# Kernel optimization log

Measured on AMD Instinct MI355X. Metric: run time of the kernel, lower is better.

The kernel has to match this reference:

```python
import jax, jax.numpy as jnp
import numpy as np

D_MODEL = 1024
N_HEAD = 16
D_HEAD = 64


def setup_inputs() -> dict:
    key = jax.random.key(0)
    k1, k2, k3 = jax.random.split(key, 3)
    B, T = 2, 2048
    x = jax.random.normal(k1, (B, T, D_MODEL), dtype=jnp.float32)
    # Linear weights (scaled like typical init to keep softmax numerics sane)
    w_attn = jax.random.normal(k2, (D_MODEL, 3 * D_MODEL), dtype=jnp.float32) * (1.0 / np.sqrt(D_MODEL))
    w_proj = jax.random.normal(k3, (D_MODEL, D_MODEL), dtype=jnp.float32) * (1.0 / np.sqrt(D_MODEL))
    return {"x": x, "w_attn": w_attn, "w_proj": w_proj}


def reference(x, w_attn, w_proj):
    B, T, C = x.shape
    # c_attn: fused qkv projection (use_bias=False)
    qkv = jnp.einsum('btc,cf->btf', x, w_attn)  # [B, T, 3C]
    q, k, v = jnp.split(qkv, 3, axis=-1)
    q = q.reshape(B, T, N_HEAD, D_HEAD)
    k = k.reshape(B, T, N_HEAD, D_HEAD)
    v = v.reshape(B, T, N_HEAD, D_HEAD)
    # scaled QK^T with causal mask (cache=None training path)
    att = jnp.einsum('bqhd,bkhd->bhqk', q, k) * (1.0 / jnp.sqrt(jnp.float32(D_HEAD)))
    causal = jnp.tril(jnp.ones((T, T), dtype=bool))  # [T, T]
    att = jnp.where(causal[None, None, :, :], att, -jnp.inf)
    att = jax.nn.softmax(att, axis=-1)
    # dropout is a no-op (deterministic / p=0)
    y = jnp.einsum('bhqk,bkhd->bqhd', att, v).reshape(B, T, C)
    y = jnp.einsum('btc,cd->btd', y, w_proj)
    return y
```

## Files before the change

kernel.cpp:

```cpp
#include <hip/hip_runtime.h>
#include <hip/hip_bf16.h>


typedef __attribute__((ext_vector_type(8))) __bf16 bf16x8;
typedef __attribute__((ext_vector_type(4))) float  floatx4;
typedef __attribute__((ext_vector_type(4))) float  fvec4;
typedef __attribute__((ext_vector_type(4))) short  short4v;

#define MFMA16(a, b, c) __builtin_amdgcn_mfma_f32_16x16x32_bf16(a, b, c, 0, 0, 0)

using as1v = const __attribute__((address_space(1))) void;
using as3v = __attribute__((address_space(3))) void;
__device__ __forceinline__ void async16(const void* g, void* l) {
  __builtin_amdgcn_global_load_lds((as1v*)g, (as3v*)l, 16, 0, 0);
}

__device__ inline void store_out(float* p, float v) { *p = v; }
__device__ inline void store_out(__hip_bfloat16* p, float v) { *p = __float2bfloat16(v); }

__global__ __launch_bounds__(256) void prep_kernel(const float* __restrict__ x,
                                                   const float* __restrict__ w_attn,
                                                   const float* __restrict__ w_proj,
                                                   __hip_bfloat16* __restrict__ xb,
                                                   __hip_bfloat16* __restrict__ wat,
                                                   __hip_bfloat16* __restrict__ wpt) {
  __shared__ float tile[32][33];
  const int bid = blockIdx.x, tid = threadIdx.x;
  if (bid < 4096) {
    const int i = (bid * 256 + tid) * 4;
    fvec4 v = *(const fvec4*)(x + i);
    union { short4v s; __hip_bfloat16 h[4]; } u;
#pragma unroll
    for (int j = 0; j < 4; ++j) u.h[j] = __float2bfloat16(v[j]);
    *(short4v*)((short*)xb + i) = u.s;
    return;
  }
  const float* in;
  __hip_bfloat16* out;
  int rows, cols, bx, by;
  if (bid < 4096 + 3072) {
    const int b2 = bid - 4096;
    in = w_attn; out = wat; rows = 1024; cols = 3072; bx = b2 % 96; by = b2 / 96;
  } else {
    const int b2 = bid - 7168;
    in = w_proj; out = wpt; rows = 1024; cols = 1024; bx = b2 % 32; by = b2 / 32;
  }
  const int tx = tid & 31, ty = tid >> 5;
  const int c0 = bx * 32, r0 = by * 32;
#pragma unroll
  for (int i = 0; i < 32; i += 8)
    tile[ty + i][tx] = in[(long)(r0 + ty + i) * cols + c0 + tx];
  __syncthreads();
#pragma unroll
  for (int i = 0; i < 32; i += 8)
    out[(long)(c0 + ty + i) * rows + r0 + tx] = __float2bfloat16(tile[tx][ty + i]);
}

__global__ __launch_bounds__(256) void vt_kernel(const __hip_bfloat16* __restrict__ qkv,
                                                 __hip_bfloat16* __restrict__ vt) {
  __shared__ __align__(16) __hip_bfloat16 tile[64 * 64];
  const int tid = threadIdx.x;
  const int tt0 = blockIdx.x * 64, h = blockIdx.y, b = blockIdx.z;
  const long bh = (long)b * 16 + h;
#pragma unroll
  for (int it = 0; it < 2; ++it) {
    const int c = it * 256 + tid;
    const int row = c >> 3, cg = c & 7;
    const int pg = cg ^ ((row >> 3) & 7);
    *(bf16x8*)(tile + row * 64 + pg * 8) =
        *(const bf16x8*)(qkv + ((long)b * 2048 + tt0 + row) * 3072 + 2048 + h * 64 + cg * 8);
  }
  __syncthreads();
#pragma unroll
  for (int it = 0; it < 2; ++it) {
    const int c = it * 256 + tid;
    const int dr = c >> 3, tg = c & 7;
    union { bf16x8 v; __hip_bfloat16 e[8]; } u;
    const int pg = (dr >> 3) ^ tg;
#pragma unroll
    for (int j = 0; j < 8; ++j)
      u.e[j] = tile[(tg * 8 + j) * 64 + pg * 8 + (dr & 7)];
    *(bf16x8*)(vt + (bh * 64 + dr) * 2048 + tt0 + tg * 8) = u.v;
  }
}

template <typename OutT>
__global__ __launch_bounds__(256) void gemm_bt_kernel(const __hip_bfloat16* __restrict__ A,
                                                      const __hip_bfloat16* __restrict__ Bt,
                                                      OutT* __restrict__ C,
                                                      int M, int N, int K,
                                                      float qscale, int qlim) {
  __shared__ __align__(16) __hip_bfloat16 As[2][128 * 32];
  __shared__ __align__(16) __hip_bfloat16 Bs[2][128 * 32];
  const int tid = threadIdx.x;
  const int lane = tid & 63, wv = tid >> 6;
  const int l15 = lane & 15, quad = lane >> 4;
  const int wm = wv >> 1, wn = wv & 1;
  const long m0 = (long)blockIdx.y * 128, n0 = (long)blockIdx.x * 128;
  floatx4 acc[4][4] = {};
  const int nk = K >> 5;

  auto issue = [&](int kt, int p) {
    const int k0 = kt << 5;
#pragma unroll
    for (int it = 0; it < 2; ++it) {
      const int c = it * 256 + tid;
      const int row = c >> 2;
      const int lcg = (c & 3) ^ ((row >> 1) & 3);
      async16(A + (m0 + row) * K + k0 + lcg * 8, (char*)&As[p][0] + c * 16);
      async16(Bt + (n0 + row) * K + k0 + lcg * 8, (char*)&Bs[p][0] + c * 16);
    }
  };

  issue(0, 0);
  for (int kt = 0; kt < nk; ++kt) {
    const int p = kt & 1;
    __syncthreads();
    if (kt + 1 < nk) issue(kt + 1, p ^ 1);
    bf16x8 af[4], bfr[4];
#pragma unroll
    for (int t = 0; t < 4; ++t) {
      const int ar = wm * 64 + t * 16 + l15;
      const int br = wn * 64 + t * 16 + l15;
      af[t]  = *(const bf16x8*)(&As[p][ar * 32 + (quad ^ ((ar >> 1) & 3)) * 8]);
      bfr[t] = *(const bf16x8*)(&Bs[p][br * 32 + (quad ^ ((br >> 1) & 3)) * 8]);
    }
#pragma unroll
    for (int mt = 0; mt < 4; ++mt)
#pragma unroll
      for (int nt = 0; nt < 4; ++nt)
        acc[mt][nt] = MFMA16(af[mt], bfr[nt], acc[mt][nt]);
  }
#pragma unroll
  for (int mt = 0; mt < 4; ++mt)
#pragma unroll
    for (int nt = 0; nt < 4; ++nt)
#pragma unroll
      for (int r = 0; r < 4; ++r) {
        const long row = m0 + wm * 64 + mt * 16 + quad * 4 + r;
        const long col = n0 + wn * 64 + nt * 16 + l15;
        float v = acc[mt][nt][r];
        if ((int)col < qlim) v *= qscale;
        store_out(C + row * N + col, v);
      }
}

template <typename OutT>
__global__ __launch_bounds__(256) void gemm_bt64_kernel(const __hip_bfloat16* __restrict__ A,
                                                        const __hip_bfloat16* __restrict__ Bt,
                                                        OutT* __restrict__ C,
                                                        int M, int N, int K) {
  __shared__ __align__(16) __hip_bfloat16 As[2][128 * 32];
  __shared__ __align__(16) __hip_bfloat16 Bs[2][64 * 32];
  const int tid = threadIdx.x;
  const int lane = tid & 63, wv = tid >> 6;
  const int l15 = lane & 15, quad = lane >> 4;
  const int wm = wv >> 1, wn = wv & 1;
  const long m0 = (long)blockIdx.y * 128, n0 = (long)blockIdx.x * 64;
  floatx4 acc[4][2] = {};
  const int nk = K >> 5;

  auto issue = [&](int kt, int p) {
    const int k0 = kt << 5;
#pragma unroll
    for (int it = 0; it < 2; ++it) {
      const int c = it * 256 + tid;
      const int row = c >> 2;
      const int lcg = (c & 3) ^ ((row >> 1) & 3);
      async16(A + (m0 + row) * K + k0 + lcg * 8, (char*)&As[p][0] + c * 16);
    }
    {
      const int c = tid;
      const int row = c >> 2;
      const int lcg = (c & 3) ^ ((row >> 1) & 3);
      async16(Bt + (n0 + row) * K + k0 + lcg * 8, (char*)&Bs[p][0] + c * 16);
    }
  };

  issue(0, 0);
  for (int kt = 0; kt < nk; ++kt) {
    const int p = kt & 1;
    __syncthreads();
    if (kt + 1 < nk) issue(kt + 1, p ^ 1);
    bf16x8 af[4], bfr[2];
#pragma unroll
    for (int t = 0; t < 4; ++t) {
      const int ar = wm * 64 + t * 16 + l15;
      af[t] = *(const bf16x8*)(&As[p][ar * 32 + (quad ^ ((ar >> 1) & 3)) * 8]);
    }
#pragma unroll
    for (int t = 0; t < 2; ++t) {
      const int br = wn * 32 + t * 16 + l15;
      bfr[t] = *(const bf16x8*)(&Bs[p][br * 32 + (quad ^ ((br >> 1) & 3)) * 8]);
    }
#pragma unroll
    for (int mt = 0; mt < 4; ++mt)
#pragma unroll
      for (int nt = 0; nt < 2; ++nt)
        acc[mt][nt] = MFMA16(af[mt], bfr[nt], acc[mt][nt]);
  }
#pragma unroll
  for (int mt = 0; mt < 4; ++mt)
#pragma unroll
    for (int nt = 0; nt < 2; ++nt)
#pragma unroll
      for (int r = 0; r < 4; ++r) {
        const long row = m0 + wm * 64 + mt * 16 + quad * 4 + r;
        const long col = n0 + wn * 32 + nt * 16 + l15;
        store_out(C + row * N + col, acc[mt][nt][r]);
      }
}

__global__ __launch_bounds__(256) void attn_kernel(const __hip_bfloat16* __restrict__ qkv,
                                                   const __hip_bfloat16* __restrict__ vtg,
                                                   __hip_bfloat16* __restrict__ y) {
  __shared__ __align__(16) __hip_bfloat16 Ks[2][64 * 64];
  __shared__ __align__(16) __hip_bfloat16 Vt[2][64 * 64];
  __shared__ __align__(16) __hip_bfloat16 Pb[4][16 * 64];
  const int tid = threadIdx.x;
  const int lane = tid & 63, wv = tid >> 6;
  const int l15 = lane & 15, quad = lane >> 4;
  const int pt = blockIdx.x, h = blockIdx.y, b = blockIdx.z;
  const int qtA = pt, qtB = 31 - pt;
  const int q0A = qtA * 64, q0B = qtB * 64;
  const long bh = (long)b * 16 + h;
  const long RS = 3072;

  auto issue = [&](int kt, int p) {
    const int kb = kt * 64;
#pragma unroll
    for (int it = 0; it < 2; ++it) {
      const int c = it * 256 + tid;
      const int row = c >> 3;
      const int cg = (c & 7) ^ (row & 7);
      async16(qkv + ((long)b * 2048 + kb + row) * RS + 1024 + h * 64 + cg * 8,
              (char*)&Ks[p][0] + c * 16);
      async16(vtg + (bh * 64 + row) * 2048 + kb + cg * 8, (char*)&Vt[p][0] + c * 16);
    }
  };

  bf16x8 bqA0, bqA1, bqB0, bqB1;
  {
    const __hip_bfloat16* qpA = qkv + ((long)b * 2048 + q0A + wv * 16 + l15) * RS + h * 64 + quad * 8;
    bqA0 = *(const bf16x8*)qpA;
    bqA1 = *(const bf16x8*)(qpA + 32);
    const __hip_bfloat16* qpB = qkv + ((long)b * 2048 + q0B + wv * 16 + l15) * RS + h * 64 + quad * 8;
    bqB0 = *(const bf16x8*)qpB;
    bqB1 = *(const bf16x8*)(qpB + 32);
  }
  union { bf16x8 v; __hip_bfloat16 e[8]; } uo;
#pragma unroll
  for (int j = 0; j < 8; ++j) uo.e[j] = __float2bfloat16(1.0f);
  const bf16x8 ones = uo.v;

  floatx4 oA[4] = {}, oB[4] = {}, o4A = {}, o4B = {};
  __hip_bfloat16* Pw = &Pb[wv][0];
  const int m7 = l15 & 7;

  issue(0, 0);
  for (int kt = 0; kt <= qtB; ++kt) {
    const int p = kt & 1;
    const int kb = kt * 64;
    const bool actA = (kt <= qtA);
    __syncthreads();
    if (kt < qtB) issue(kt + 1, p ^ 1);

    bf16x8 kf[4][2], vf[4][2];
#pragma unroll
    for (int nt = 0; nt < 4; ++nt) {
      const int row = nt * 16 + l15;
      const int s0 = (quad ^ (row & 7)) * 8, s1 = ((quad + 4) ^ (row & 7)) * 8;
      kf[nt][0] = *(const bf16x8*)(&Ks[p][row * 64 + s0]);
      kf[nt][1] = *(const bf16x8*)(&Ks[p][row * 64 + s1]);
      vf[nt][0] = *(const bf16x8*)(&Vt[p][row * 64 + s0]);
      vf[nt][1] = *(const bf16x8*)(&Vt[p][row * 64 + s1]);
    }

    auto tile = [&](const bf16x8& bq0, const bf16x8& bq1, floatx4* o, floatx4& o4,
                    bool diag, int q0X) {
      floatx4 st[4] = {};
#pragma unroll
      for (int nt = 0; nt < 4; ++nt) {
        st[nt] = MFMA16(kf[nt][0], bq0, st[nt]);
        st[nt] = MFMA16(kf[nt][1], bq1, st[nt]);
      }
      const int qg = q0X + wv * 16 + l15;
#pragma unroll
      for (int nt = 0; nt < 4; ++nt) {
        union { short4v s; __hip_bfloat16 h[4]; } up;
#pragma unroll
        for (int r = 0; r < 4; ++r) {
          float pv = exp2f(st[nt][r]);
          if (diag && (kb + nt * 16 + quad * 4 + r > qg)) pv = 0.f;
          up.h[r] = __float2bfloat16(pv);
        }
        const int chunk = (nt * 2 + (quad >> 1)) ^ m7;
        *(short4v*)(Pw + l15 * 64 + chunk * 8 + (quad & 1) * 4) = up.s;
      }
      const bf16x8 pb0 = *(const bf16x8*)(Pw + l15 * 64 + (quad ^ m7) * 8);
      const bf16x8 pb1 = *(const bf16x8*)(Pw + l15 * 64 + ((quad + 4) ^ m7) * 8);
#pragma unroll
      for (int mt = 0; mt < 4; ++mt) {
        o[mt] = MFMA16(vf[mt][0], pb0, o[mt]);
        o[mt] = MFMA16(vf[mt][1], pb1, o[mt]);
      }
      o4 = MFMA16(ones, pb0, o4);
      o4 = MFMA16(ones, pb1, o4);
    };

    tile(bqB0, bqB1, oB, o4B, kt == qtB, q0B);
    if (actA) tile(bqA0, bqA1, oA, o4A, kt == qtA, q0A);
  }

  auto epi = [&](floatx4* o, floatx4& o4, int q0X) {
    const float inv = 1.0f / o4[0];
    const long t = (long)b * 2048 + q0X + wv * 16 + l15;
#pragma unroll
    for (int mt = 0; mt < 4; ++mt) {
      union { short4v s; __hip_bfloat16 h[4]; } uy;
#pragma unroll
      for (int r = 0; r < 4; ++r) uy.h[r] = __float2bfloat16(o[mt][r] * inv);
      *(short4v*)(y + t * 1024 + h * 64 + mt * 16 + quad * 4) = uy.s;
    }
  };
  epi(oA, o4A, q0A);
  epi(oB, o4B, q0B);
}

extern "C" void kernel_launch(void* const* d_in, const int* in_sizes, int n_in,
                              void* d_out, int out_size, void* d_ws, size_t ws_size,
                              hipStream_t stream) {
  const float* x      = (const float*)d_in[0];
  const float* w_attn = (const float*)d_in[1];
  const float* w_proj = (const float*)d_in[2];
  float* out = (float*)d_out;
  char* ws = (char*)d_ws;
  __hip_bfloat16* xb   = (__hip_bfloat16*)(ws);
  __hip_bfloat16* wat  = (__hip_bfloat16*)(ws + 8388608);
  __hip_bfloat16* qkvb = (__hip_bfloat16*)(ws + 16777216);
  __hip_bfloat16* wpt  = (__hip_bfloat16*)(ws + 41943040);
  __hip_bfloat16* vtg  = xb;
  __hip_bfloat16* yb   = wat;
  const float SC = 0.18033688011112042f;

  prep_kernel<<<8192, 256, 0, stream>>>(x, w_attn, w_proj, xb, wat, wpt);
  gemm_bt_kernel<__hip_bfloat16><<<dim3(24, 32), 256, 0, stream>>>(xb, wat, qkvb, 4096, 3072, 1024, SC, 1024);
  vt_kernel<<<dim3(32, 16, 2), 256, 0, stream>>>(qkvb, vtg);
  attn_kernel<<<dim3(16, 16, 2), 256, 0, stream>>>(qkvb, vtg, yb);
  gemm_bt64_kernel<float><<<dim3(16, 32), 256, 0, stream>>>(yb, wpt, out, 4096, 1024, 1024);
}
```

Baseline: 186.1 us.

## Fuse V transpose into QKV GEMM epilogue and vectorize weight transpose-convert

The QKV GEMM epilogue now writes Q and K into a narrower 2048-column buffer and writes V directly in transposed per-head layout, so the separate vt_kernel launch and its extra read and write of V go away. The weight prep kernel switches to 64x64 tiles with vectorized float4 loads, bf16 conversion before staging in shared memory, a swizzled tile, and 16-byte stores. The attention kernel's row stride changes to match the new Q/K buffer. The transposed V stores from the GEMM are 8-byte writes strided by 2048 elements, which may coalesce less well than the old dedicated transpose.

```diff
diff --git a/kernel.cpp b/kernel.cpp
--- a/kernel.cpp
+++ b/kernel.cpp
@@ -24,7 +24,6 @@
                                                    __hip_bfloat16* __restrict__ xb,
                                                    __hip_bfloat16* __restrict__ wat,
                                                    __hip_bfloat16* __restrict__ wpt) {
-  __shared__ float tile[32][33];
   const int bid = blockIdx.x, tid = threadIdx.x;
   if (bid < 4096) {
     const int i = (bid * 256 + tid) * 4;
@@ -35,40 +34,29 @@
     *(short4v*)((short*)xb + i) = u.s;
     return;
   }
+  __shared__ __align__(16) __hip_bfloat16 tile[64 * 64];
   const float* in;
   __hip_bfloat16* out;
-  int rows, cols, bx, by;
-  if (bid < 4096 + 3072) {
+  int cols, bx, by;
+  if (bid < 4864) {
     const int b2 = bid - 4096;
-    in = w_attn; out = wat; rows = 1024; cols = 3072; bx = b2 % 96; by = b2 / 96;
+    in = w_attn; out = wat; cols = 3072; bx = b2 % 48; by = b2 / 48;
   } else {
-    const int b2 = bid - 7168;
-    in = w_proj; out = wpt; rows = 1024; cols = 1024; bx = b2 % 32; by = b2 / 32;
-  }
-  const int tx = tid & 31, ty = tid >> 5;
-  const int c0 = bx * 32, r0 = by * 32;
-#pragma unroll
-  for (int i = 0; i < 32; i += 8)
-    tile[ty + i][tx] = in[(long)(r0 + ty + i) * cols + c0 + tx];
-  __syncthreads();
-#pragma unroll
-  for (int i = 0; i < 32; i += 8)
-    out[(long)(c0 + ty + i) * rows + r0 + tx] = __float2bfloat16(tile[tx][ty + i]);
-}
-
-__global__ __launch_bounds__(256) void vt_kernel(const __hip_bfloat16* __restrict__ qkv,
-                                                 __hip_bfloat16* __restrict__ vt) {
-  __shared__ __align__(16) __hip_bfloat16 tile[64 * 64];
-  const int tid = threadIdx.x;
-  const int tt0 = blockIdx.x * 64, h = blockIdx.y, b = blockIdx.z;
-  const long bh = (long)b * 16 + h;
+    const int b2 = bid - 4864;
+    in = w_proj; out = wpt; cols = 1024; bx = b2 % 16; by = b2 / 16;
+  }
+  const int c0 = bx * 64, r0 = by * 64;
 #pragma unroll
   for (int it = 0; it < 2; ++it) {
     const int c = it * 256 + tid;
     const int row = c >> 3, cg = c & 7;
-    const int pg = cg ^ ((row >> 3) & 7);
-    *(bf16x8*)(tile + row * 64 + pg * 8) =
-        *(const bf16x8*)(qkv + ((long)b * 2048 + tt0 + row) * 3072 + 2048 + h * 64 + cg * 8);
+    const float* src = in + (long)(r0 + row) * cols + c0 + cg * 8;
+    fvec4 v0 = *(const fvec4*)src;
+    fvec4 v1 = *(const fvec4*)(src + 4);
+    union { bf16x8 v; __hip_bfloat16 h[8]; } u;
+#pragma unroll
+    for (int j = 0; j < 4; ++j) { u.h[j] = __float2bfloat16(v0[j]); u.h[4 + j] = __float2bfloat16(v1[j]); }
+    *(bf16x8*)(tile + row * 64 + (cg ^ ((row >> 3) & 7)) * 8) = u.v;
   }
   __syncthreads();
 #pragma unroll
@@ -80,16 +68,16 @@
 #pragma unroll
     for (int j = 0; j < 8; ++j)
       u.e[j] = tile[(tg * 8 + j) * 64 + pg * 8 + (dr & 7)];
-    *(bf16x8*)(vt + (bh * 64 + dr) * 2048 + tt0 + tg * 8) = u.v;
-  }
-}
-
-template <typename OutT>
-__global__ __launch_bounds__(256) void gemm_bt_kernel(const __hip_bfloat16* __restrict__ A,
-                                                      const __hip_bfloat16* __restrict__ Bt,
-                                                      OutT* __restrict__ C,
-                                                      int M, int N, int K,
-                                                      float qscale, int qlim) {
+    *(bf16x8*)(out + (long)(c0 + dr) * 1024 + r0 + tg * 8) = u.v;
+  }
+}
+
+__global__ __launch_bounds__(256) void gemm_qkv_kernel(const __hip_bfloat16* __restrict__ A,
+                                                       const __hip_bfloat16* __restrict__ Bt,
+                                                       __hip_bfloat16* __restrict__ qk,
+                                                       __hip_bfloat16* __restrict__ vt,
+                                                       float qscale) {
+  const int K = 1024;
   __shared__ __align__(16) __hip_bfloat16 As[2][128 * 32];
   __shared__ __align__(16) __hip_bfloat16 Bs[2][128 * 32];
   const int tid = threadIdx.x;
@@ -131,18 +119,35 @@
       for (int nt = 0; nt < 4; ++nt)
         acc[mt][nt] = MFMA16(af[mt], bfr[nt], acc[mt][nt]);
   }
-#pragma unroll
-  for (int mt = 0; mt < 4; ++mt)
-#pragma unroll
-    for (int nt = 0; nt < 4; ++nt)
-#pragma unroll
-      for (int r = 0; r < 4; ++r) {
-        const long row = m0 + wm * 64 + mt * 16 + quad * 4 + r;
-        const long col = n0 + wn * 64 + nt * 16 + l15;
-        float v = acc[mt][nt][r];
-        if ((int)col < qlim) v *= qscale;
-        store_out(C + row * N + col, v);
-      }
+
+#pragma unroll
+  for (int nt = 0; nt < 4; ++nt) {
+    const int colb = (int)n0 + wn * 64 + nt * 16;
+    if (colb >= 2048) {
+      const int hh = (colb - 2048) >> 6;
+      const int d  = (colb & 63) + l15;
+#pragma unroll
+      for (int mt = 0; mt < 4; ++mt) {
+        const long row = m0 + wm * 64 + mt * 16 + quad * 4;
+        const long b   = row >> 11;
+        const long t0  = row & 2047;
+        union { short4v s; __hip_bfloat16 h[4]; } uy;
+#pragma unroll
+        for (int r = 0; r < 4; ++r) uy.h[r] = __float2bfloat16(acc[mt][nt][r]);
+        *(short4v*)(vt + ((b * 16 + hh) * 64 + d) * 2048 + t0) = uy.s;
+      }
+    } else {
+      const float sc = (colb < 1024) ? qscale : 1.0f;
+      const long col = colb + l15;
+#pragma unroll
+      for (int mt = 0; mt < 4; ++mt)
+#pragma unroll
+        for (int r = 0; r < 4; ++r) {
+          const long row = m0 + wm * 64 + mt * 16 + quad * 4 + r;
+          qk[row * 2048 + col] = __float2bfloat16(acc[mt][nt][r] * sc);
+        }
+    }
+  }
 }
 
 template <typename OutT>
@@ -211,7 +216,7 @@
       }
 }
 
-__global__ __launch_bounds__(256) void attn_kernel(const __hip_bfloat16* __restrict__ qkv,
+__global__ __launch_bounds__(256) void attn_kernel(const __hip_bfloat16* __restrict__ qk,
                                                    const __hip_bfloat16* __restrict__ vtg,
                                                    __hip_bfloat16* __restrict__ y) {
   __shared__ __align__(16) __hip_bfloat16 Ks[2][64 * 64];
@@ -224,7 +229,7 @@
   const int qtA = pt, qtB = 31 - pt;
   const int q0A = qtA * 64, q0B = qtB * 64;
   const long bh = (long)b * 16 + h;
-  const long RS = 3072;
+  const long RS = 2048;
 
   auto issue = [&](int kt, int p) {
     const int kb = kt * 64;
@@ -233,7 +238,7 @@
       const int c = it * 256 + tid;
       const int row = c >> 3;
       const int cg = (c & 7) ^ (row & 7);
-      async16(qkv + ((long)b * 2048 + kb + row) * RS + 1024 + h * 64 + cg * 8,
+      async16(qk + ((long)b * 2048 + kb + row) * RS + 1024 + h * 64 + cg * 8,
               (char*)&Ks[p][0] + c * 16);
       async16(vtg + (bh * 64 + row) * 2048 + kb + cg * 8, (char*)&Vt[p][0] + c * 16);
     }
@@ -241,10 +246,10 @@
 
   bf16x8 bqA0, bqA1, bqB0, bqB1;
   {
-    const __hip_bfloat16* qpA = qkv + ((long)b * 2048 + q0A + wv * 16 + l15) * RS + h * 64 + quad * 8;
+    const __hip_bfloat16* qpA = qk + ((long)b * 2048 + q0A + wv * 16 + l15) * RS + h * 64 + quad * 8;
     bqA0 = *(const bf16x8*)qpA;
     bqA1 = *(const bf16x8*)(qpA + 32);
-    const __hip_bfloat16* qpB = qkv + ((long)b * 2048 + q0B + wv * 16 + l15) * RS + h * 64 + quad * 8;
+    const __hip_bfloat16* qpB = qk + ((long)b * 2048 + q0B + wv * 16 + l15) * RS + h * 64 + quad * 8;
     bqB0 = *(const bf16x8*)qpB;
     bqB1 = *(const bf16x8*)(qpB + 32);
   }
@@ -335,17 +340,16 @@
   const float* w_proj = (const float*)d_in[2];
   float* out = (float*)d_out;
   char* ws = (char*)d_ws;
-  __hip_bfloat16* xb   = (__hip_bfloat16*)(ws);
-  __hip_bfloat16* wat  = (__hip_bfloat16*)(ws + 8388608);
-  __hip_bfloat16* qkvb = (__hip_bfloat16*)(ws + 16777216);
-  __hip_bfloat16* wpt  = (__hip_bfloat16*)(ws + 41943040);
-  __hip_bfloat16* vtg  = xb;
-  __hip_bfloat16* yb   = wat;
+  __hip_bfloat16* xb  = (__hip_bfloat16*)(ws);
+  __hip_bfloat16* wat = (__hip_bfloat16*)(ws + 8388608);
+  __hip_bfloat16* qk  = (__hip_bfloat16*)(ws + 16777216);
+  __hip_bfloat16* wpt = (__hip_bfloat16*)(ws + 33554432);
+  __hip_bfloat16* vtg = (__hip_bfloat16*)(ws + 35651584);
+  __hip_bfloat16* yb  = wat;
   const float SC = 0.18033688011112042f;
 
-  prep_kernel<<<8192, 256, 0, stream>>>(x, w_attn, w_proj, xb, wat, wpt);
-  gemm_bt_kernel<__hip_bfloat16><<<dim3(24, 32), 256, 0, stream>>>(xb, wat, qkvb, 4096, 3072, 1024, SC, 1024);
-  vt_kernel<<<dim3(32, 16, 2), 256, 0, stream>>>(qkvb, vtg);
-  attn_kernel<<<dim3(16, 16, 2), 256, 0, stream>>>(qkvb, vtg, yb);
+  prep_kernel<<<5120, 256, 0, stream>>>(x, w_attn, w_proj, xb, wat, wpt);
+  gemm_qkv_kernel<<<dim3(24, 32), 256, 0, stream>>>(xb, wat, qk, vtg, SC);
+  attn_kernel<<<dim3(16, 16, 2), 256, 0, stream>>>(qk, vtg, yb);
   gemm_bt64_kernel<float><<<dim3(16, 32), 256, 0, stream>>>(yb, wpt, out, 4096, 1024, 1024);
 }
```

After: 182.0 us. 2.2% less time.
